# Optimization experiments

Measured on AMD Instinct MI355X. Metric: run time of the kernel, lower is better.

Reference implementation:

```python
import jax, jax.numpy as jnp
import numpy as np

B, N, K = 8, 2048, 100  # graphs per batch, nodes per graph, diffpool clusters


def _bn(x, g, b, eps=1e-5):
    # BatchNorm1d in training mode over all B*N nodes (biased variance)
    m = x.mean(axis=(0, 1))
    v = x.var(axis=(0, 1))
    return (x - m) * jax.lax.rsqrt(v + eps) * g + b


def _norm_adj(A):
    # PyG gcn_norm: add remaining self-loops (fill=1), D^-1/2 (A+I) D^-1/2
    n = A.shape[-1]
    d = jnp.diagonal(A, axis1=-2, axis2=-1)
    A_hat = A + jnp.where(d == 0, 1.0, 0.0)[..., :, None] * jnp.eye(n, dtype=A.dtype)
    deg = A_hat.sum(-1)
    dinv = jnp.where(deg > 0, 1.0 / jnp.sqrt(deg), 0.0)
    return dinv[..., :, None] * A_hat * dinv[..., None, :]


def _gcn(An, x, W, b):
    # GCNConv: propagate(x @ W) + bias, with pre-normalized adjacency
    return An @ (x @ W) + b


def _forward(x, adj, W_in, W3030, Wp13, b30, b100, Wfc_pool, bfc_pool,
             W1, b1, W2, b2, gamma30, beta30, gamma100, beta100):
    A_w = _norm_adj(adj)                               # weighted (edge_attr) adjacency
    A_b = _norm_adj((adj > 0).astype(adj.dtype))       # pool convs ignore edge_attr
    # feature branch
    x11 = _bn(_gcn(A_w, x, W_in[0], b30[0]), gamma30[0], beta30[0])
    x12 = _bn(_gcn(A_w, x11, W3030[0], b30[1]), gamma30[1], beta30[1])
    x13 = _bn(_gcn(A_w, x12, W3030[1], b30[2]), gamma30[2], beta30[2])
    x1_out = jnp.concatenate([x11, x12, x13], -1).max(axis=1)   # [B,90]
    # assignment branch
    s11 = _bn(_gcn(A_b, x, W_in[1], b30[3]), gamma30[3], beta30[3])
    s12 = _bn(_gcn(A_b, s11, W3030[2], b30[4]), gamma30[4], beta30[4])
    s13 = _bn(_gcn(A_b, s12, Wp13, b100), gamma100, beta100)
    s1 = jnp.concatenate([s11, s12, s13], -1) @ Wfc_pool + bfc_pool  # [B,N,K]
    # dense_diff_pool (link/entropy losses are unused by the forward output)
    s = jax.nn.softmax(s1, -1)
    p1_x = jnp.einsum('bnk,bnd->bkd', s, x13)          # s^T x  [B,K,30]
    p1_adj = jnp.einsum('bnk,bnl->bkl', s, adj @ s)    # s^T A s  [B,K,K]
    # second stage on pooled (dense, weighted) graph
    A2 = _norm_adj(p1_adj)
    x21 = _bn(_gcn(A2, p1_x, W3030[3], b30[5]), gamma30[5], beta30[5])
    x22 = _bn(_gcn(A2, x21, W3030[4], b30[6]), gamma30[6], beta30[6])
    x23 = _bn(_gcn(A2, x22, W3030[5], b30[7]), gamma30[7], beta30[7])
    x2_out = jnp.concatenate([x21, x22, x23], -1).max(axis=1)   # [B,90]
    h = jnp.concatenate([x1_out, x2_out], -1) @ W1 + b1
    return jax.nn.relu(h) @ W2 + b2                    # [B,6]


def setup_inputs():
    key = jax.random.key(0)
    ks = jax.random.split(key, 12)
    u = jax.random.uniform(ks[0], (B, N, N), dtype=jnp.float32)
    mask = jax.random.uniform(ks[1], (B, N, N)) < 0.05
    A = jnp.triu(u * mask, 1)
    adj = A + jnp.swapaxes(A, -1, -2)
    x = jax.random.normal(ks[2], (B, N, 3), dtype=jnp.float32)
    w = lambda k, s: jax.random.normal(k, s, dtype=jnp.float32) * 0.1
    return dict(
        x=x, adj=adj,
        W_in=w(ks[3], (2, 3, 30)),      # conv11, pool_conv11
        W3030=w(ks[4], (6, 30, 30)),    # conv12, conv13, pool_conv12, conv21..23
        Wp13=w(ks[5], (30, 100)),
        b30=jnp.zeros((8, 30), jnp.float32),
        b100=jnp.zeros((100,), jnp.float32),
        Wfc_pool=w(ks[6], (160, 100)), bfc_pool=jnp.zeros((100,), jnp.float32),
        W1=w(ks[7], (180, 50)), b1=jnp.zeros((50,), jnp.float32),
        W2=w(ks[8], (50, 6)), b2=jnp.zeros((6,), jnp.float32),
        gamma30=jnp.ones((8, 30), jnp.float32), beta30=jnp.zeros((8, 30), jnp.float32),
        gamma100=jnp.ones((100,), jnp.float32), beta100=jnp.zeros((100,), jnp.float32),
    )


def reference(x, adj, W_in, W3030, Wp13, b30, b100, Wfc_pool, bfc_pool,
              W1, b1, W2, b2, gamma30, beta30, gamma100, beta100):
    return _forward(x, adj, W_in, W3030, Wp13, b30, b100, Wfc_pool, bfc_pool,
                    W1, b1, W2, b2, gamma30, beta30, gamma100, beta100)
```

## Files before the change

kernel.cpp:

```cpp
#include <hip/hip_runtime.h>
#include <hip/hip_fp16.h>
#include <cstdint>
#include <cstddef>

#define BATCH 8
#define NN 2048
#define RTOT 16384
#define CAP 176

static constexpr size_t OF_B1W   = 0;
static constexpr size_t OF_B1B   = 3840;
static constexpr size_t OF_B2W   = 7680;
static constexpr size_t OF_B2B   = 11520;
static constexpr size_t OF_B3W   = 15360;
static constexpr size_t OF_B3B   = 15840;
static constexpr size_t OF_S2    = 17440;
static constexpr size_t OF_CNT   = 17620;
static constexpr size_t ZEND     = 17632;
static constexpr size_t OF_ELLV  = 17664;
static constexpr size_t OF_ELLC  = OF_ELLV + 2883584;
static constexpr size_t OF_ROWLEN= OF_ELLC + 1441792;
static constexpr size_t OF_DINVW = OF_ROWLEN + 16384;
static constexpr size_t OF_DINVB = OF_DINVW + 16384;
static constexpr size_t OF_HWB   = OF_DINVB + 16384;
static constexpr size_t OF_HW3   = OF_HWB + 524288;
static constexpr size_t OF_HB100 = OF_HW3 + 262144;
static constexpr size_t OF_ZW    = OF_HB100 + 851968;
static constexpr size_t OF_ZB    = OF_ZW + 524288;
static constexpr size_t OF_X11   = OF_ZB + 1703936;
static constexpr size_t OF_X12   = OF_X11 + 524288;
static constexpr size_t OF_X13   = OF_X12 + 524288;
static constexpr size_t OF_S11   = OF_X13 + 524288;
static constexpr size_t OF_S12   = OF_S11 + 524288;
static constexpr size_t OF_PARTMAX = OF_S12 + 524288;

#define FMA4(acc, s, h) { acc.x += (s)*(h).x; acc.y += (s)*(h).y; acc.z += (s)*(h).z; acc.w += (s)*(h).w; }

__device__ __forceinline__ unsigned short f2h(float f) {
  _Float16 h = (_Float16)f;
  return *(unsigned short*)&h;
}
__device__ __forceinline__ float h2f(unsigned short s) {
  _Float16 h = *(_Float16*)&s;
  return (float)h;
}
__device__ __forceinline__ float2 h2f2(unsigned int u) {
  __half2 h = *(__half2*)&u;
  return __half22float2(h);
}

struct __align__(8) us4 { unsigned short x, y, z, w; };

#define ACC8(g, wt) { \
  float2 f0=h2f2((g).x), f1=h2f2((g).y), f2=h2f2((g).z), f3=h2f2((g).w); \
  acc[0] += (wt)*f0.x; acc[1] += (wt)*f0.y; acc[2] += (wt)*f1.x; acc[3] += (wt)*f1.y; \
  acc[4] += (wt)*f2.x; acc[5] += (wt)*f2.y; acc[6] += (wt)*f3.x; acc[7] += (wt)*f3.y; }


__global__ __launch_bounds__(256) void k_build_ell(
    const float* __restrict__ adj, const float* __restrict__ x,
    const float* __restrict__ Win, float* __restrict__ ellv,
    unsigned short* __restrict__ ellc, int* __restrict__ rowlen,
    float* __restrict__ dinvw, float* __restrict__ dinvb,
    unsigned short* __restrict__ Hwb, float* __restrict__ zbase)
{
  int r = blockIdx.x;
  int t = threadIdx.x, lane = t & 63, wv = t >> 6;
  if (blockIdx.x < 69) {
    int zi = blockIdx.x * 256 + t;
    if (zi < (int)ZEND) zbase[zi] = 0.f;
  }
  const float* row = adj + (size_t)r * NN;
  __shared__ int wcnt[4];
  __shared__ float wsumA[4];
  __shared__ float dsh[2];
  float4 a = ((const float4*)row)[t];
  float4 b = ((const float4*)row)[256 + t];
  float vals[8] = {a.x, a.y, a.z, a.w, b.x, b.y, b.z, b.w};
  int cbase0 = t*4, cbase1 = 1024 + t*4;
  int cnt = 0; float sum = 0.f;
#pragma unroll
  for (int k = 0; k < 8; ++k) { sum += vals[k]; cnt += (vals[k] != 0.f) ? 1 : 0; }
  int pre = cnt;
#pragma unroll
  for (int o = 1; o < 64; o <<= 1) { int n = __shfl_up(pre, o); if (lane >= o) pre += n; }
  int excl = pre - cnt;
  int wtot = __shfl(pre, 63);
#pragma unroll
  for (int o = 32; o; o >>= 1) sum += __shfl_down(sum, o);
  if (lane == 0) { wcnt[wv] = wtot; wsumA[wv] = sum; }
  __syncthreads();
  int base = 0;
  for (int w = 0; w < wv; ++w) base += wcnt[w];
  int p = base + excl;
  size_t rb = (size_t)r * CAP;
#pragma unroll
  for (int k = 0; k < 8; ++k) {
    float v = vals[k];
    if (v != 0.f && p < CAP) {
      ellv[rb + p] = v;
      ellc[rb + p] = (unsigned short)((k < 4) ? (cbase0 + k) : (cbase1 + (k - 4)));
      ++p;
    }
  }
  if (t == 0) {
    int tot = wcnt[0] + wcnt[1] + wcnt[2] + wcnt[3];
    float ws = wsumA[0] + wsumA[1] + wsumA[2] + wsumA[3];
    int nnz = tot < CAP ? tot : CAP;
    int n = nnz;
    while ((n & 3) && n < CAP) { ellv[rb + n] = 0.f; ellc[rb + n] = 0; ++n; }
    rowlen[r] = n;
    float dw = rsqrtf(ws + 1.f), db = rsqrtf((float)nnz + 1.f);
    dinvw[r] = dw; dinvb[r] = db;
    dsh[0] = dw; dsh[1] = db;
  }
  __syncthreads();
  if (t < 64) {
    int c = t & 31, side = t >> 5;
    float v = 0.f;
    if (c < 30) {
      float x0 = x[r*3], x1 = x[r*3+1], x2 = x[r*3+2];
      const float* W = Win + side*90;
      v = (x0*W[c] + x1*W[30+c] + x2*W[60+c]) * dsh[side];
    }
    Hwb[(size_t)r*64 + t] = f2h(v);
  }
}

__global__ __launch_bounds__(256) void k_spmm_pair(
    const unsigned short* __restrict__ Hwb, const float* __restrict__ ellv,
    const unsigned short* __restrict__ ellc, const int* __restrict__ rowlen,
    const float* __restrict__ dinvw, const float* __restrict__ dinvb,
    float* __restrict__ Zw, float* __restrict__ Zb,
    float* __restrict__ bktW, float* __restrict__ bktB)
{
  __shared__ float zsW[32][32];
  __shared__ float zsB[32][32];
  int t = threadIdx.x;
  int gid = blockIdx.x * 256 + t;
  int row = gid >> 3, q = gid & 7;
  int side = q >> 2, sub = q & 3;
  int len = rowlen[row];
  const float4* ev = (const float4*)(ellv + (size_t)row * CAP);
  const uint2*  ec = (const uint2*) (ellc + (size_t)row * CAP);
  const uint4* HP = (const uint4*)(Hwb + (size_t)(row >> 11) * (NN*64));
  float acc[8] = {0,0,0,0,0,0,0,0};
  int nit = len >> 2;
  for (int i = 0; i < nit; ++i) {
    float4 v = ev[i];
    uint2 cc = ec[i];
    int c0 = cc.x & 0xffff, c1 = cc.x >> 16, c2 = cc.y & 0xffff, c3 = cc.y >> 16;
    uint4 g0 = HP[c0*8+q], g1 = HP[c1*8+q], g2 = HP[c2*8+q], g3 = HP[c3*8+q];
    float w0 = side ? (v.x>0.f?1.f:0.f) : v.x;
    float w1 = side ? (v.y>0.f?1.f:0.f) : v.y;
    float w2 = side ? (v.z>0.f?1.f:0.f) : v.z;
    float w3 = side ? (v.w>0.f?1.f:0.f) : v.w;
    ACC8(g0, w0); ACC8(g1, w1); ACC8(g2, w2); ACC8(g3, w3);
  }
  uint4 hs = HP[(row & (NN-1))*8 + q];
  ACC8(hs, 1.f);
  float d = side ? dinvb[row] : dinvw[row];
#pragma unroll
  for (int k = 0; k < 8; ++k) acc[k] *= d;
  float* Zp = (side ? Zb : Zw) + (size_t)row*32 + sub*8;
  float4 o0 = {acc[0],acc[1],acc[2],acc[3]}, o1 = {acc[4],acc[5],acc[6],acc[7]};
  ((float4*)Zp)[0] = o0; ((float4*)Zp)[1] = o1;
  int rowloc = t >> 3;
  float (*zs)[32] = side ? zsB : zsW;
#pragma unroll
  for (int k = 0; k < 8; ++k) zs[rowloc][sub*8+k] = acc[k];
  __syncthreads();
  int copy = blockIdx.x & 63;
  if (t < 30) {
    float s1 = 0.f, s2 = 0.f;
    for (int r = 0; r < 32; ++r) { float v = zsW[r][t]; s1 += v; s2 += v*v; }
    atomicAdd(&bktW[(t*64+copy)*2],   s1);
    atomicAdd(&bktW[(t*64+copy)*2+1], s2);
  } else if (t >= 64 && t < 94) {
    int c = t - 64;
    float s1 = 0.f, s2 = 0.f;
    for (int r = 0; r < 32; ++r) { float v = zsB[r][c]; s1 += v; s2 += v*v; }
    atomicAdd(&bktB[(c*64+copy)*2],   s1);
    atomicAdd(&bktB[(c*64+copy)*2+1], s2);
  }
}

__global__ __launch_bounds__(256) void k_spmm_l3(
    const unsigned short* __restrict__ Hw3, const unsigned short* __restrict__ Hb100,
    const float* __restrict__ ellv, const unsigned short* __restrict__ ellc,
    const int* __restrict__ rowlen, const float* __restrict__ dinvw,
    const float* __restrict__ dinvb, float* __restrict__ Zw, float* __restrict__ Zb,
    float* __restrict__ bktW3, float* __restrict__ bktB3)
{
  __shared__ float zs[64][32];
  __shared__ float st[200];
  int t = threadIdx.x;
  if (blockIdx.x < 256) {
    int gid = blockIdx.x * 256 + t;
    int row = gid >> 2, q = gid & 3;
    int len = rowlen[row];
    const float4* ev = (const float4*)(ellv + (size_t)row * CAP);
    const uint2*  ec = (const uint2*) (ellc + (size_t)row * CAP);
    const uint4* HP = (const uint4*)(Hw3 + (size_t)(row >> 11) * (NN*32));
    float acc[8] = {0,0,0,0,0,0,0,0};
    int nit = len >> 2;
    for (int i = 0; i < nit; ++i) {
      float4 v = ev[i];
      uint2 cc = ec[i];
      int c0 = cc.x & 0xffff, c1 = cc.x >> 16, c2 = cc.y & 0xffff, c3 = cc.y >> 16;
      uint4 g0 = HP[c0*4+q], g1 = HP[c1*4+q], g2 = HP[c2*4+q], g3 = HP[c3*4+q];
      ACC8(g0, v.x); ACC8(g1, v.y); ACC8(g2, v.z); ACC8(g3, v.w);
    }
    uint4 hs = HP[(row & (NN-1))*4 + q];
    ACC8(hs, 1.f);
    float d = dinvw[row];
#pragma unroll
    for (int k = 0; k < 8; ++k) acc[k] *= d;
    float* Zp = Zw + (size_t)row*32 + q*8;
    float4 o0 = {acc[0],acc[1],acc[2],acc[3]}, o1 = {acc[4],acc[5],acc[6],acc[7]};
    ((float4*)Zp)[0] = o0; ((float4*)Zp)[1] = o1;
    int rowloc = t >> 2;
#pragma unroll
    for (int k = 0; k < 8; ++k) zs[rowloc][q*8+k] = acc[k];
    __syncthreads();
    if (t < 30) {
      float s1 = 0.f, s2 = 0.f;
      for (int r = 0; r < 64; ++r) { float v = zs[r][t]; s1 += v; s2 += v*v; }
      int copy = blockIdx.x & 7;
      atomicAdd(&bktW3[(t*8+copy)*2],   s1);
      atomicAdd(&bktW3[(t*8+copy)*2+1], s2);
    }
  } else {
    int bid = blockIdx.x - 256;
    for (int i = t; i < 200; i += 256) st[i] = 0.f;
    __syncthreads();
    int gid = bid * 256 + t;
    int row = gid / 13, q = gid - row*13;
    int len = rowlen[row];
    const float4* ev = (const float4*)(ellv + (size_t)row * CAP);
    const uint2*  ec = (const uint2*) (ellc + (size_t)row * CAP);
    const uint4* HP = (const uint4*)(Hb100 + (size_t)(row >> 11) * ((size_t)NN*104));
    float acc[8] = {0,0,0,0,0,0,0,0};
    int nit = len >> 2;
    for (int i = 0; i < nit; ++i) {
      float4 v = ev[i];
      uint2 cc = ec[i];
      int c0 = cc.x & 0xffff, c1 = cc.x >> 16, c2 = cc.y & 0xffff, c3 = cc.y >> 16;
      uint4 g0 = HP[c0*13+q], g1 = HP[c1*13+q], g2 = HP[c2*13+q], g3 = HP[c3*13+q];
      float w0 = (v.x>0.f?1.f:0.f), w1 = (v.y>0.f?1.f:0.f);
      float w2 = (v.z>0.f?1.f:0.f), w3 = (v.w>0.f?1.f:0.f);
      ACC8(g0, w0); ACC8(g1, w1); ACC8(g2, w2); ACC8(g3, w3);
    }
    uint4 hs = HP[(row & (NN-1))*13 + q];
    ACC8(hs, 1.f);
    float d = dinvb[row];
#pragma unroll
    for (int k = 0; k < 8; ++k) acc[k] *= d;
    float* Zp = Zb + (size_t)row*104 + q*8;
    float4 o0 = {acc[0],acc[1],acc[2],acc[3]}, o1 = {acc[4],acc[5],acc[6],acc[7]};
    ((float4*)Zp)[0] = o0; ((float4*)Zp)[1] = o1;
    int c0 = q*8;
#pragma unroll
    for (int k = 0; k < 8; ++k) {
      int ch = c0 + k;
      if (ch < 100) { atomicAdd(&st[ch*2], acc[k]); atomicAdd(&st[ch*2+1], acc[k]*acc[k]); }
    }
    __syncthreads();
    int copy = bid & 7;
    for (int i = t; i < 200; i += 256)
      atomicAdd(&bktB3[((i>>1)*8 + copy)*2 + (i&1)], st[i]);
  }
}

template<int LEVEL>
__global__ __launch_bounds__(256) void k_apply_gemm(
    const float* __restrict__ Zw, const float* __restrict__ bktW,
    const float* __restrict__ gW, const float* __restrict__ beW,
    float* __restrict__ xst, const float* __restrict__ Ww,
    const float* __restrict__ dinvw,
    const float* __restrict__ Zb, const float* __restrict__ bktB,
    const float* __restrict__ gB, const float* __restrict__ beB,
    float* __restrict__ sst, const float* __restrict__ Wb,
    const float* __restrict__ dinvb,
    unsigned short* __restrict__ HwOut, unsigned short* __restrict__ HbOut)
{
  constexpr int NGB = (LEVEL == 1) ? 8 : 26;
  constexpr int OSTRIDEB = (LEVEL == 1) ? 32 : 104;
  constexpr int NG = 8 + NGB;
  __shared__ float WwL[30*32];
  __shared__ float WbL[30*OSTRIDEB];
  __shared__ float awL[60], abL[60];
  int t = threadIdx.x;
  if (t < 60) {
    int c = t % 30;
    bool isW = t < 30;
    const float4* p = (const float4*)((isW ? bktW : bktB) + c*128);
    float s1 = 0.f, s2 = 0.f;
#pragma unroll
    for (int k = 0; k < 32; ++k) { float4 v = p[k]; s1 += v.x + v.z; s2 += v.y + v.w; }
    float mean = s1/16384.f, var = s2/16384.f - mean*mean, inv = rsqrtf(var + 1e-5f);
    float aa = (isW ? gW : gB)[c]*inv;
    float* dst = isW ? awL : abL;
    dst[c] = aa; dst[30+c] = (isW ? beW : beB)[c] - mean*aa;
  }
  for (int idx = t; idx < 30*32; idx += 256) {
    int k = idx >> 5, c = idx & 31;
    WwL[idx] = (c < 30) ? Ww[k*30 + c] : 0.f;
  }
  if (LEVEL == 1) {
    for (int idx = t; idx < 30*32; idx += 256) {
      int k = idx >> 5, c = idx & 31;
      WbL[idx] = (c < 30) ? Wb[k*30 + c] : 0.f;
    }
  } else {
    for (int idx = t; idx < 30*OSTRIDEB; idx += 256) {
      int k = idx / OSTRIDEB, j = idx % OSTRIDEB;
      WbL[idx] = (j < 100) ? Wb[k*100 + j] : 0.f;
    }
  }
  __syncthreads();
  int gid = blockIdx.x * 256 + t;
  int row = gid / NG, g = gid % NG;
  if (g < 8) {
    const float4* Z4 = (const float4*)Zw + (size_t)row*8;
    float4 z4[8];
#pragma unroll
    for (int u = 0; u < 8; ++u) z4[u] = Z4[u];
    const float* z = (const float*)z4;
    float4 xv;
    int ch = 4*g;
    xv.x = (ch+0 < 30) ? awL[ch+0]*z[ch+0] + awL[30+ch+0] : 0.f;
    xv.y = (ch+1 < 30) ? awL[ch+1]*z[ch+1] + awL[30+ch+1] : 0.f;
    xv.z = (ch+2 < 30) ? awL[ch+2]*z[ch+2] + awL[30+ch+2] : 0.f;
    xv.w = (ch+3 < 30) ? awL[ch+3]*z[ch+3] + awL[30+ch+3] : 0.f;
    ((float4*)xst)[(size_t)row*8+g] = xv;
    float4 o = {0,0,0,0};
#pragma unroll
    for (int k = 0; k < 30; ++k) {
      float xk = awL[k]*z[k] + awL[30+k];
      float4 w = *(const float4*)(WwL + k*32 + 4*g);
      FMA4(o, xk, w);
    }
    float d = dinvw[row];
    us4 pv = { f2h(d*o.x), f2h(d*o.y), f2h(d*o.z), f2h(d*o.w) };
    unsigned short* dst = (LEVEL == 1) ? (HwOut + (size_t)row*64 + 4*g)
                                       : (HwOut + (size_t)row*32 + 4*g);
    *(us4*)dst = pv;
  } else {
    int gb = g - 8;
    const float4* Z4 = (const float4*)Zb + (size_t)row*8;
    float4 z4[8];
#pragma unroll
    for (int u = 0; u < 8; ++u) z4[u] = Z4[u];
    const float* z = (const float*)z4;
    if (gb < 8) {
      int ch = 4*gb;
      float4 sv;
      sv.x = (ch+0 < 30) ? abL[ch+0]*z[ch+0] + abL[30+ch+0] : 0.f;
      sv.y = (ch+1 < 30) ? abL[ch+1]*z[ch+1] + abL[30+ch+1] : 0.f;
      sv.z = (ch+2 < 30) ? abL[ch+2]*z[ch+2] + abL[30+ch+2] : 0.f;
      sv.w = (ch+3 < 30) ? abL[ch+3]*z[ch+3] + abL[30+ch+3] : 0.f;
      ((float4*)sst)[(size_t)row*8+gb] = sv;
    }
    float4 o = {0,0,0,0};
#pragma unroll
    for (int k = 0; k < 30; ++k) {
      float sk = abL[k]*z[k] + abL[30+k];
      float4 w = *(const float4*)(WbL + k*OSTRIDEB + 4*gb);
      FMA4(o, sk, w);
    }
    float d = dinvb[row];
    us4 pv = { f2h(d*o.x), f2h(d*o.y), f2h(d*o.z), f2h(d*o.w) };
    unsigned short* dst = (LEVEL == 1) ? (HbOut + (size_t)row*64 + 32 + 4*gb)
                                       : (HbOut + (size_t)row*104 + 4*gb);
    *(us4*)dst = pv;
  }
}

__global__ __launch_bounds__(256) void k_fcpool(
    const float* __restrict__ Zw3, const float* __restrict__ bktW3,
    const float* __restrict__ gW3, const float* __restrict__ beW3,
    const float* __restrict__ Zb3, const float* __restrict__ bktB3,
    const float* __restrict__ g100, const float* __restrict__ be100,
    const float* __restrict__ s11, const float* __restrict__ s12,
    const float* __restrict__ Wfc, const float* __restrict__ bfc,
    float* __restrict__ x13, unsigned short* __restrict__ S)
{
  __shared__ float shm[14240];
  __shared__ float aw3[60], ab3[200];
  float* feat = shm;
  float* Wl = shm + 10240;
  int t = threadIdx.x;
  int g0 = blockIdx.x * 64;
  if (t < 30) {
    const float4* p = (const float4*)(bktW3 + t*16);
    float s1 = 0.f, s2 = 0.f;
#pragma unroll
    for (int k = 0; k < 4; ++k) { float4 v = p[k]; s1 += v.x + v.z; s2 += v.y + v.w; }
    float mean = s1/16384.f, var = s2/16384.f - mean*mean, inv = rsqrtf(var + 1e-5f);
    float aa = gW3[t]*inv; aw3[t] = aa; aw3[30+t] = beW3[t] - mean*aa;
  } else if (t >= 64 && t < 164) {
    int c = t - 64;
    const float4* p = (const float4*)(bktB3 + c*16);
    float s1 = 0.f, s2 = 0.f;
#pragma unroll
    for (int k = 0; k < 4; ++k) { float4 v = p[k]; s1 += v.x + v.z; s2 += v.y + v.w; }
    float mean = s1/16384.f, var = s2/16384.f - mean*mean, inv = rsqrtf(var + 1e-5f);
    float aa = g100[c]*inv; ab3[c] = aa; ab3[100+c] = be100[c] - mean*aa;
  }
  __syncthreads();
  for (int idx = t; idx < 64*160; idx += 256) {
    int l = idx / 160, c = idx % 160;
    int g = g0 + l;
    float v;
    if (c < 30) v = s11[(size_t)g*32 + c];
    else if (c < 60) v = s12[(size_t)g*32 + (c-30)];
    else { int k = c - 60; v = ab3[k]*Zb3[(size_t)g*104 + k] + ab3[100 + k]; }
    feat[l*160 + c] = v;
  }
  for (int idx = t; idx < 64*32; idx += 256) {
    int l = idx >> 5, c = idx & 31;
    int g = g0 + l;
    x13[(size_t)g*32+c] = (c < 30) ? aw3[c]*Zw3[(size_t)g*32+c] + aw3[30+c] : 0.f;
  }
  int np = t >> 3, kg = t & 7;
  int n0 = np*2, n1 = np*2 + 1;
  int kbase = kg*12 + (kg < 4 ? kg : 4);
  int klen  = kg < 4 ? 13 : 12;
  float a0[13], a1[13];
#pragma unroll
  for (int j = 0; j < 13; ++j) { a0[j] = 0.f; a1[j] = 0.f; }
  for (int ch = 0; ch < 4; ++ch) {
    __syncthreads();
    for (int idx = t; idx < 4000; idx += 256) {
      int r = idx/100, j = idx%100;
      Wl[r*100 + j] = Wfc[(ch*40 + r)*100 + j];
    }
    __syncthreads();
    for (int kk = 0; kk < 40; ++kk) {
      float f0 = feat[n0*160 + ch*40+kk];
      float f1 = feat[n1*160 + ch*40+kk];
#pragma unroll
      for (int j = 0; j < 13; ++j) {
        if (j < klen) {
          float w = Wl[kk*100 + kbase + j];
          a0[j] += f0*w; a1[j] += f1*w;
        }
      }
    }
  }
  __syncthreads();
  float* sRow = shm;
  for (int j = 0; j < klen; ++j) {
    int k = kbase + j;
    sRow[n0*100 + k] = a0[j] + bfc[k];
    sRow[n1*100 + k] = a1[j] + bfc[k];
  }
  __syncthreads();
  int n = t >> 2, part = t & 3;
  int i0 = part*25;
  float m = -3.4e38f;
  for (int i = 0; i < 25; ++i) m = fmaxf(m, sRow[n*100 + i0 + i]);
  m = fmaxf(m, __shfl_xor(m, 1));
  m = fmaxf(m, __shfl_xor(m, 2));
  float ev[25]; float s = 0.f;
  for (int i = 0; i < 25; ++i) { float e = __expf(sRow[n*100 + i0 + i] - m); ev[i] = e; s += e; }
  s += __shfl_xor(s, 1);
  s += __shfl_xor(s, 2);
  float rinv = 1.f / s;
  for (int i = 0; i < 25; ++i) S[(size_t)(g0+n)*104 + i0 + i] = f2h(ev[i] * rinv);
  if (part == 3) {
    S[(size_t)(g0+n)*104 + 100] = 0; S[(size_t)(g0+n)*104 + 101] = 0;
    S[(size_t)(g0+n)*104 + 102] = 0; S[(size_t)(g0+n)*104 + 103] = 0;
  }
}

__global__ __launch_bounds__(256) void k_spmm_as(
    const unsigned short* __restrict__ S, const float* __restrict__ ellv,
    const unsigned short* __restrict__ ellc, const int* __restrict__ rowlen,
    float* __restrict__ Z)
{
  int t = threadIdx.x;
  int gid = blockIdx.x * 256 + t;
  int row = gid / 13, q = gid - row*13;
  int len = rowlen[row];
  const float4* ev = (const float4*)(ellv + (size_t)row * CAP);
  const uint2*  ec = (const uint2*) (ellc + (size_t)row * CAP);
  const uint4* HP = (const uint4*)(S + (size_t)(row >> 11) * ((size_t)NN*104));
  float acc[8] = {0,0,0,0,0,0,0,0};
  int nit = len >> 2;
  for (int i = 0; i < nit; ++i) {
    float4 v = ev[i];
    uint2 cc = ec[i];
    int c0 = cc.x & 0xffff, c1 = cc.x >> 16, c2 = cc.y & 0xffff, c3 = cc.y >> 16;
    uint4 g0 = HP[c0*13+q], g1 = HP[c1*13+q], g2 = HP[c2*13+q], g3 = HP[c3*13+q];
    ACC8(g0, v.x); ACC8(g1, v.y); ACC8(g2, v.z); ACC8(g3, v.w);
  }
  float* Zp = Z + (size_t)row*104 + q*8;
  float4 o0 = {acc[0],acc[1],acc[2],acc[3]}, o1 = {acc[4],acc[5],acc[6],acc[7]};
  ((float4*)Zp)[0] = o0; ((float4*)Zp)[1] = o1;
}

__global__ __launch_bounds__(256) void k_pool_part(
    const unsigned short* __restrict__ S, const float* __restrict__ x13,
    const float* __restrict__ As, const float* __restrict__ x11,
    const float* __restrict__ x12, float* __restrict__ pp, float* __restrict__ pm)
{
  __shared__ float sL[64][100];
  __shared__ float xL[64][132];
  __shared__ float red[256];
  int t = threadIdx.x;
  int b = blockIdx.x >> 3, chunk = blockIdx.x & 7;
  int g00 = b * 2048 + chunk * 256;
  int kt = t/10, dt = t%10;
  int k0 = kt*4, d0 = dt*13;
  float acc[4][13];
#pragma unroll
  for (int a = 0; a < 4; ++a)
#pragma unroll
    for (int j = 0; j < 13; ++j) acc[a][j] = 0.f;
  for (int tile = 0; tile < 4; ++tile) {
    int g0 = g00 + tile*64;
    __syncthreads();
    for (int idx = t; idx < 64*100; idx += 256) {
      int l = idx/100, k = idx%100;
      sL[l][k] = h2f(S[(size_t)(g0+l)*104 + k]);
    }
    for (int idx = t; idx < 64*130; idx += 256) {
      int l = idx/130, d = idx%130;
      xL[l][d] = d < 30 ? x13[(size_t)(g0+l)*32 + d] : As[(size_t)(g0+l)*104 + (d-30)];
    }
    __syncthreads();
    if (t < 250) {
      for (int kk = 0; kk < 64; ++kk) {
        float sv[4];
#pragma unroll
        for (int a = 0; a < 4; ++a) sv[a] = sL[kk][k0+a];
#pragma unroll
        for (int j = 0; j < 13; ++j) {
          float xv = xL[kk][d0+j];
#pragma unroll
          for (int a = 0; a < 4; ++a) acc[a][j] += sv[a]*xv;
        }
      }
    }
  }
  if (t < 250) {
    float* dst = pp + (size_t)blockIdx.x * 13000;
    for (int a = 0; a < 4; ++a)
      for (int j = 0; j < 13; ++j)
        dst[(k0+a)*130 + (d0+j)] = acc[a][j];
  }
  __syncthreads();
  {
    int c = t & 31, rg = t >> 5;
    const float* srcs[3] = {x11, x12, x13};
    for (int a = 0; a < 3; ++a) {
      const float* p = srcs[a] + (size_t)(g00+rg)*32 + c;
      float m = -3.4e38f;
      for (int it = 0; it < 32; ++it) m = fmaxf(m, p[it*256]);
      red[t] = m;
      __syncthreads();
      if (t < 30) {
        float mm = red[t];
        for (int g = 1; g < 8; ++g) mm = fmaxf(mm, red[g*32+t]);
        pm[(size_t)blockIdx.x*90 + a*30 + t] = mm;
      }
      __syncthreads();
    }
  }
}

__global__ __launch_bounds__(256) void k_s2fused(
    const float* __restrict__ pp, const float* __restrict__ partmax,
    const float* __restrict__ Wm,
    const float* __restrict__ g30,
    const float* __restrict__ be30,
    float* __restrict__ bktS2,
    int* __restrict__ cnt,
    const float* __restrict__ W1, const float* __restrict__ b1,
    const float* __restrict__ W2, const float* __restrict__ b2,
    float* __restrict__ out)
{
  __shared__ float A2f[10000];
  __shared__ float buf1[3000];
  __shared__ float buf2[3200];
  __shared__ float WL[960];
  __shared__ float dl[100];
  __shared__ float st1[30], st2[30];
  __shared__ float coef[60];
  __shared__ float x1L[90], x2L[90], hh[50];
  int b = blockIdx.x, t = threadIdx.x;
  for (int idx = t; idx < 13000; idx += 256) {
    float s = 0.f;
    for (int ch = 0; ch < 8; ++ch) s += pp[(size_t)(b*8 + ch)*13000 + idx];
    int k = idx/130, d = idx%130;
    if (d < 30) buf1[k*30 + d] = s;
    else A2f[k*100 + (d-30)] = s;
  }
  __syncthreads();
  if (t < 100 && A2f[t*101] == 0.f) A2f[t*101] = 1.f;
  __syncthreads();
  if (t < 100) {
    float s = 0.f;
    for (int j = 0; j < 100; ++j) s += A2f[t*100 + j];
    dl[t] = s > 0.f ? rsqrtf(s) : 0.f;
  }
  __syncthreads();
  for (int idx = t; idx < 10000; idx += 256) {
    int i = idx/100, j = idx%100;
    A2f[idx] = dl[i]*dl[j]*A2f[idx];
  }
  int rp = t >> 2, cg = t & 3;
  int i0 = rp*2, c0 = cg*8;
  bool act = (t < 200);
  for (int L = 0; L < 3; ++L) {
    if (t < 30) { st1[t] = 0.f; st2[t] = 0.f; }
    const float* W = Wm + L*900;
    for (int idx = t; idx < 960; idx += 256) {
      int k = idx >> 5, c = idx & 31;
      WL[idx] = (c < 30) ? W[k*30 + c] : 0.f;
    }
    __syncthreads();
    if (act) {
      float a0[8] = {0,0,0,0,0,0,0,0}, a1[8] = {0,0,0,0,0,0,0,0};
      for (int k = 0; k < 30; ++k) {
        float xx0 = buf1[i0*30 + k], xx1 = buf1[(i0+1)*30 + k];
        float4 w0 = *(const float4*)&WL[k*32 + c0];
        float4 w1 = *(const float4*)&WL[k*32 + c0 + 4];
        a0[0] += xx0*w0.x; a0[1] += xx0*w0.y; a0[2] += xx0*w0.z; a0[3] += xx0*w0.w;
        a0[4] += xx0*w1.x; a0[5] += xx0*w1.y; a0[6] += xx0*w1.z; a0[7] += xx0*w1.w;
        a1[0] += xx1*w0.x; a1[1] += xx1*w0.y; a1[2] += xx1*w0.z; a1[3] += xx1*w0.w;
        a1[4] += xx1*w1.x; a1[5] += xx1*w1.y; a1[6] += xx1*w1.z; a1[7] += xx1*w1.w;
      }
      float4 s00 = {a0[0],a0[1],a0[2],a0[3]}, s01 = {a0[4],a0[5],a0[6],a0[7]};
      float4 s10 = {a1[0],a1[1],a1[2],a1[3]}, s11v = {a1[4],a1[5],a1[6],a1[7]};
      *(float4*)&buf2[i0*32 + c0]       = s00;
      *(float4*)&buf2[i0*32 + c0 + 4]   = s01;
      *(float4*)&buf2[(i0+1)*32 + c0]   = s10;
      *(float4*)&buf2[(i0+1)*32 + c0+4] = s11v;
    }
    __syncthreads();
    if (act) {
      float z0[8] = {0,0,0,0,0,0,0,0}, z1[8] = {0,0,0,0,0,0,0,0};
      for (int j = 0; j < 100; ++j) {
        float av0 = A2f[i0*100 + j], av1 = A2f[(i0+1)*100 + j];
        float4 t0 = *(const float4*)&buf2[j*32 + c0];
        float4 t1 = *(const float4*)&buf2[j*32 + c0 + 4];
        z0[0] += av0*t0.x; z0[1] += av0*t0.y; z0[2] += av0*t0.z; z0[3] += av0*t0.w;
        z0[4] += av0*t1.x; z0[5] += av0*t1.y; z0[6] += av0*t1.z; z0[7] += av0*t1.w;
        z1[0] += av1*t0.x; z1[1] += av1*t0.y; z1[2] += av1*t0.z; z1[3] += av1*t0.w;
        z1[4] += av1*t1.x; z1[5] += av1*t1.y; z1[6] += av1*t1.z; z1[7] += av1*t1.w;
      }
#pragma unroll
      for (int k = 0; k < 8; ++k) {
        int c = c0 + k;
        if (c < 30) {
          buf1[i0*30 + c]     = z0[k];
          buf1[(i0+1)*30 + c] = z1[k];
          atomicAdd(&st1[c], z0[k] + z1[k]);
          atomicAdd(&st2[c], z0[k]*z0[k] + z1[k]*z1[k]);
        }
      }
    }
    __syncthreads();
    if (t < 30) {
      atomicAdd(&bktS2[(L*30+t)*2],   st1[t]);
      atomicAdd(&bktS2[(L*30+t)*2+1], st2[t]);
    }
    __syncthreads();
    if (t == 0) {
      __threadfence();
      atomicAdd(cnt, 1);
      while (atomicAdd(cnt, 0) < (L+1)*8) {}
      __threadfence();
    }
    __syncthreads();
    if (t < 30) {
      float s1 = atomicAdd(&bktS2[(L*30+t)*2],   0.f);
      float s2 = atomicAdd(&bktS2[(L*30+t)*2+1], 0.f);
      float mean = s1/800.f, var = s2/800.f - mean*mean, inv = rsqrtf(var + 1e-5f);
      float aa = g30[L*30+t]*inv;
      coef[t] = aa; coef[30+t] = be30[L*30+t] - mean*aa;
    }
    __syncthreads();
    if (L < 2) {
      for (int idx = t; idx < 3000; idx += 256) {
        int c = idx % 30;
        buf1[idx] = coef[c]*buf1[idx] + coef[30+c];
      }
      __syncthreads();
      if (t < 30) {
        float m = -3.4e38f;
        for (int i = 0; i < 100; ++i) m = fmaxf(m, buf1[i*30+t]);
        x2L[L*30+t] = m;
      }
      __syncthreads();
    } else {
      if (t < 30) {
        float m = -3.4e38f;
        for (int i = 0; i < 100; ++i) m = fmaxf(m, coef[t]*buf1[i*30+t] + coef[30+t]);
        x2L[60+t] = m;
      }
    }
  }
  if (t < 90) {
    float m = -3.4e38f;
    for (int s = 0; s < 8; ++s) m = fmaxf(m, partmax[(size_t)(b*8+s)*90 + t]);
    x1L[t] = m;
  }
  __syncthreads();
  if (t < 50) {
    float a = b1[t];
    for (int k = 0; k < 90; ++k) a += x1L[k]*W1[k*50+t];
    for (int k = 0; k < 90; ++k) a += x2L[k]*W1[(90+k)*50+t];
    hh[t] = fmaxf(a, 0.f);
  }
  __syncthreads();
  if (t < 6) {
    float a = b2[t];
    for (int j = 0; j < 50; ++j) a += hh[j]*W2[j*6+t];
    out[b*6+t] = a;
  }
}

extern "C" void kernel_launch(void* const* d_in, const int* in_sizes, int n_in,
                              void* d_out, int out_size, void* d_ws, size_t ws_size,
                              hipStream_t stream)
{
  const float* x    = (const float*)d_in[0];
  const float* adj  = (const float*)d_in[1];
  const float* Win  = (const float*)d_in[2];
  const float* W3030= (const float*)d_in[3];
  const float* Wp13 = (const float*)d_in[4];
  const float* Wfc  = (const float*)d_in[7];
  const float* bfc  = (const float*)d_in[8];
  const float* W1   = (const float*)d_in[9];
  const float* b1   = (const float*)d_in[10];
  const float* W2   = (const float*)d_in[11];
  const float* b2   = (const float*)d_in[12];
  const float* g30  = (const float*)d_in[13];
  const float* be30 = (const float*)d_in[14];
  const float* g100 = (const float*)d_in[15];
  const float* be100= (const float*)d_in[16];
  float* out = (float*)d_out;

  float* wsf = (float*)d_ws;
  float* bL1W = wsf + OF_B1W;  float* bL1B = wsf + OF_B1B;
  float* bL2W = wsf + OF_B2W;  float* bL2B = wsf + OF_B2B;
  float* bL3W = wsf + OF_B3W;  float* bL3B = wsf + OF_B3B;
  float* bktS2 = wsf + OF_S2;
  int*   cnt  = (int*)(wsf + OF_CNT);
  float* ellv  = wsf + OF_ELLV;
  unsigned short* ellc = (unsigned short*)(wsf + OF_ELLC);
  int*   rowlen = (int*)(wsf + OF_ROWLEN);
  float* dinvw = wsf + OF_DINVW;
  float* dinvb = wsf + OF_DINVB;
  unsigned short* Hwb   = (unsigned short*)(wsf + OF_HWB);
  unsigned short* Hw3   = (unsigned short*)(wsf + OF_HW3);
  unsigned short* Hb100 = (unsigned short*)(wsf + OF_HB100);
  unsigned short* S     = Hb100;
  float* Zw = wsf + OF_ZW;
  float* Zb = wsf + OF_ZB;
  float* x11 = wsf + OF_X11;
  float* x12 = wsf + OF_X12;
  float* x13 = wsf + OF_X13;
  float* s11 = wsf + OF_S11;
  float* s12 = wsf + OF_S12;
  float* pp  = wsf + OF_S11;
  float* partmax = wsf + OF_PARTMAX;

  k_build_ell<<<RTOT, 256, 0, stream>>>(adj, x, Win, ellv, ellc, rowlen, dinvw, dinvb, Hwb, wsf);

  k_spmm_pair<<<512, 256, 0, stream>>>(Hwb, ellv, ellc, rowlen, dinvw, dinvb, Zw, Zb, bL1W, bL1B);
  k_apply_gemm<1><<<1024, 256, 0, stream>>>(Zw, bL1W, g30+0, be30+0, x11, W3030+0, dinvw,
                                            Zb, bL1B, g30+90, be30+90, s11, W3030+2*900, dinvb, Hwb, Hwb);

  k_spmm_pair<<<512, 256, 0, stream>>>(Hwb, ellv, ellc, rowlen, dinvw, dinvb, Zw, Zb, bL2W, bL2B);
  k_apply_gemm<2><<<2176, 256, 0, stream>>>(Zw, bL2W, g30+30, be30+30, x12, W3030+900, dinvw,
                                            Zb, bL2B, g30+120, be30+120, s12, Wp13, dinvb, Hw3, Hb100);

  k_spmm_l3<<<1088, 256, 0, stream>>>(Hw3, Hb100, ellv, ellc, rowlen, dinvw, dinvb, Zw, Zb, bL3W, bL3B);
  k_fcpool<<<256, 256, 0, stream>>>(Zw, bL3W, g30+60, be30+60, Zb, bL3B, g100, be100,
                                    s11, s12, Wfc, bfc, x13, S);

  k_spmm_as<<<832, 256, 0, stream>>>(S, ellv, ellc, rowlen, Zb );
  k_pool_part<<<64, 256, 0, stream>>>(S, x13, Zb, x11, x12, pp, partmax);

  k_s2fused<<<BATCH, 256, 0, stream>>>(pp, partmax, W3030+3*900, g30+150, be30+150,
                                       bktS2, cnt, W1, b1, W2, b2, out);
}
```

Baseline: 658.9 us.

## Split pooling into more blocks with separate reduce kernel, unroll SpMM gathers by two

The pooling partial-product kernel now uses 256 blocks of 64 rows each instead of 64 blocks looping over four tiles. This fills more compute units, and a new reduction kernel sums the 32 partials per graph before the final fused kernel. The SpMM gather loops in several kernels are unrolled by two to keep eight independent gathers in flight. The cost is an extra launch, a larger partials buffer in the workspace, and higher register pressure.

```diff
diff --git a/kernel.cpp b/kernel.cpp
--- a/kernel.cpp
+++ b/kernel.cpp
@@ -33,6 +33,8 @@
 static constexpr size_t OF_S11   = OF_X13 + 524288;
 static constexpr size_t OF_S12   = OF_S11 + 524288;
 static constexpr size_t OF_PARTMAX = OF_S12 + 524288;
+static constexpr size_t OF_PP    = OF_PARTMAX + 23040;
+static constexpr size_t OF_PPOOL = OF_PP + 3328000;
 
 #define FMA4(acc, s, h) { acc.x += (s)*(h).x; acc.y += (s)*(h).y; acc.z += (s)*(h).z; acc.w += (s)*(h).w; }
 
@@ -146,7 +148,26 @@
   const uint4* HP = (const uint4*)(Hwb + (size_t)(row >> 11) * (NN*64));
   float acc[8] = {0,0,0,0,0,0,0,0};
   int nit = len >> 2;
-  for (int i = 0; i < nit; ++i) {
+  int i = 0;
+  for (; i + 2 <= nit; i += 2) {
+    float4 v0 = ev[i], v1 = ev[i+1];
+    uint2 cc0 = ec[i], cc1 = ec[i+1];
+    int a0 = cc0.x & 0xffff, a1 = cc0.x >> 16, a2 = cc0.y & 0xffff, a3 = cc0.y >> 16;
+    int e0 = cc1.x & 0xffff, e1 = cc1.x >> 16, e2 = cc1.y & 0xffff, e3 = cc1.y >> 16;
+    uint4 g0 = HP[a0*8+q], g1 = HP[a1*8+q], g2 = HP[a2*8+q], g3 = HP[a3*8+q];
+    uint4 g4 = HP[e0*8+q], g5 = HP[e1*8+q], g6 = HP[e2*8+q], g7 = HP[e3*8+q];
+    float w0 = side ? (v0.x>0.f?1.f:0.f) : v0.x;
+    float w1 = side ? (v0.y>0.f?1.f:0.f) : v0.y;
+    float w2 = side ? (v0.z>0.f?1.f:0.f) : v0.z;
+    float w3 = side ? (v0.w>0.f?1.f:0.f) : v0.w;
+    float w4 = side ? (v1.x>0.f?1.f:0.f) : v1.x;
+    float w5 = side ? (v1.y>0.f?1.f:0.f) : v1.y;
+    float w6 = side ? (v1.z>0.f?1.f:0.f) : v1.z;
+    float w7 = side ? (v1.w>0.f?1.f:0.f) : v1.w;
+    ACC8(g0, w0); ACC8(g1, w1); ACC8(g2, w2); ACC8(g3, w3);
+    ACC8(g4, w4); ACC8(g5, w5); ACC8(g6, w6); ACC8(g7, w7);
+  }
+  if (i < nit) {
     float4 v = ev[i];
     uint2 cc = ec[i];
     int c0 = cc.x & 0xffff, c1 = cc.x >> 16, c2 = cc.y & 0xffff, c3 = cc.y >> 16;
@@ -204,7 +225,18 @@
     const uint4* HP = (const uint4*)(Hw3 + (size_t)(row >> 11) * (NN*32));
     float acc[8] = {0,0,0,0,0,0,0,0};
     int nit = len >> 2;
-    for (int i = 0; i < nit; ++i) {
+    int i = 0;
+    for (; i + 2 <= nit; i += 2) {
+      float4 v0 = ev[i], v1 = ev[i+1];
+      uint2 cc0 = ec[i], cc1 = ec[i+1];
+      int a0 = cc0.x & 0xffff, a1 = cc0.x >> 16, a2 = cc0.y & 0xffff, a3 = cc0.y >> 16;
+      int e0 = cc1.x & 0xffff, e1 = cc1.x >> 16, e2 = cc1.y & 0xffff, e3 = cc1.y >> 16;
+      uint4 g0 = HP[a0*4+q], g1 = HP[a1*4+q], g2 = HP[a2*4+q], g3 = HP[a3*4+q];
+      uint4 g4 = HP[e0*4+q], g5 = HP[e1*4+q], g6 = HP[e2*4+q], g7 = HP[e3*4+q];
+      ACC8(g0, v0.x); ACC8(g1, v0.y); ACC8(g2, v0.z); ACC8(g3, v0.w);
+      ACC8(g4, v1.x); ACC8(g5, v1.y); ACC8(g6, v1.z); ACC8(g7, v1.w);
+    }
+    if (i < nit) {
       float4 v = ev[i];
       uint2 cc = ec[i];
       int c0 = cc.x & 0xffff, c1 = cc.x >> 16, c2 = cc.y & 0xffff, c3 = cc.y >> 16;
@@ -242,7 +274,22 @@
     const uint4* HP = (const uint4*)(Hb100 + (size_t)(row >> 11) * ((size_t)NN*104));
     float acc[8] = {0,0,0,0,0,0,0,0};
     int nit = len >> 2;
-    for (int i = 0; i < nit; ++i) {
+    int i = 0;
+    for (; i + 2 <= nit; i += 2) {
+      float4 v0 = ev[i], v1 = ev[i+1];
+      uint2 cc0 = ec[i], cc1 = ec[i+1];
+      int a0 = cc0.x & 0xffff, a1 = cc0.x >> 16, a2 = cc0.y & 0xffff, a3 = cc0.y >> 16;
+      int e0 = cc1.x & 0xffff, e1 = cc1.x >> 16, e2 = cc1.y & 0xffff, e3 = cc1.y >> 16;
+      uint4 g0 = HP[a0*13+q], g1 = HP[a1*13+q], g2 = HP[a2*13+q], g3 = HP[a3*13+q];
+      uint4 g4 = HP[e0*13+q], g5 = HP[e1*13+q], g6 = HP[e2*13+q], g7 = HP[e3*13+q];
+      float w0 = (v0.x>0.f?1.f:0.f), w1 = (v0.y>0.f?1.f:0.f);
+      float w2 = (v0.z>0.f?1.f:0.f), w3 = (v0.w>0.f?1.f:0.f);
+      float w4 = (v1.x>0.f?1.f:0.f), w5 = (v1.y>0.f?1.f:0.f);
+      float w6 = (v1.z>0.f?1.f:0.f), w7 = (v1.w>0.f?1.f:0.f);
+      ACC8(g0, w0); ACC8(g1, w1); ACC8(g2, w2); ACC8(g3, w3);
+      ACC8(g4, w4); ACC8(g5, w5); ACC8(g6, w6); ACC8(g7, w7);
+    }
+    if (i < nit) {
       float4 v = ev[i];
       uint2 cc = ec[i];
       int c0 = cc.x & 0xffff, c1 = cc.x >> 16, c2 = cc.y & 0xffff, c3 = cc.y >> 16;
@@ -267,8 +314,8 @@
     }
     __syncthreads();
     int copy = bid & 7;
-    for (int i = t; i < 200; i += 256)
-      atomicAdd(&bktB3[((i>>1)*8 + copy)*2 + (i&1)], st[i]);
+    for (int i2 = t; i2 < 200; i2 += 256)
+      atomicAdd(&bktB3[((i2>>1)*8 + copy)*2 + (i2&1)], st[i2]);
   }
 }
 
@@ -327,12 +374,13 @@
 #pragma unroll
     for (int u = 0; u < 8; ++u) z4[u] = Z4[u];
     const float* z = (const float*)z4;
+    int ch = 4*g;
+    float4 zg = Z4[g];
     float4 xv;
-    int ch = 4*g;
-    xv.x = (ch+0 < 30) ? awL[ch+0]*z[ch+0] + awL[30+ch+0] : 0.f;
-    xv.y = (ch+1 < 30) ? awL[ch+1]*z[ch+1] + awL[30+ch+1] : 0.f;
-    xv.z = (ch+2 < 30) ? awL[ch+2]*z[ch+2] + awL[30+ch+2] : 0.f;
-    xv.w = (ch+3 < 30) ? awL[ch+3]*z[ch+3] + awL[30+ch+3] : 0.f;
+    xv.x = (ch+0 < 30) ? awL[ch+0]*zg.x + awL[30+ch+0] : 0.f;
+    xv.y = (ch+1 < 30) ? awL[ch+1]*zg.y + awL[30+ch+1] : 0.f;
+    xv.z = (ch+2 < 30) ? awL[ch+2]*zg.z + awL[30+ch+2] : 0.f;
+    xv.w = (ch+3 < 30) ? awL[ch+3]*zg.w + awL[30+ch+3] : 0.f;
     ((float4*)xst)[(size_t)row*8+g] = xv;
     float4 o = {0,0,0,0};
 #pragma unroll
@@ -355,11 +403,12 @@
     const float* z = (const float*)z4;
     if (gb < 8) {
       int ch = 4*gb;
+      float4 zg = Z4[gb];
       float4 sv;
-      sv.x = (ch+0 < 30) ? abL[ch+0]*z[ch+0] + abL[30+ch+0] : 0.f;
-      sv.y = (ch+1 < 30) ? abL[ch+1]*z[ch+1] + abL[30+ch+1] : 0.f;
-      sv.z = (ch+2 < 30) ? abL[ch+2]*z[ch+2] + abL[30+ch+2] : 0.f;
-      sv.w = (ch+3 < 30) ? abL[ch+3]*z[ch+3] + abL[30+ch+3] : 0.f;
+      sv.x = (ch+0 < 30) ? abL[ch+0]*zg.x + abL[30+ch+0] : 0.f;
+      sv.y = (ch+1 < 30) ? abL[ch+1]*zg.y + abL[30+ch+1] : 0.f;
+      sv.z = (ch+2 < 30) ? abL[ch+2]*zg.z + abL[30+ch+2] : 0.f;
+      sv.w = (ch+3 < 30) ? abL[ch+3]*zg.w + abL[30+ch+3] : 0.f;
       ((float4*)sst)[(size_t)row*8+gb] = sv;
     }
     float4 o = {0,0,0,0};
@@ -489,7 +538,18 @@
   const uint4* HP = (const uint4*)(S + (size_t)(row >> 11) * ((size_t)NN*104));
   float acc[8] = {0,0,0,0,0,0,0,0};
   int nit = len >> 2;
-  for (int i = 0; i < nit; ++i) {
+  int i = 0;
+  for (; i + 2 <= nit; i += 2) {
+    float4 v0 = ev[i], v1 = ev[i+1];
+    uint2 cc0 = ec[i], cc1 = ec[i+1];
+    int a0 = cc0.x & 0xffff, a1 = cc0.x >> 16, a2 = cc0.y & 0xffff, a3 = cc0.y >> 16;
+    int e0 = cc1.x & 0xffff, e1 = cc1.x >> 16, e2 = cc1.y & 0xffff, e3 = cc1.y >> 16;
+    uint4 g0 = HP[a0*13+q], g1 = HP[a1*13+q], g2 = HP[a2*13+q], g3 = HP[a3*13+q];
+    uint4 g4 = HP[e0*13+q], g5 = HP[e1*13+q], g6 = HP[e2*13+q], g7 = HP[e3*13+q];
+    ACC8(g0, v0.x); ACC8(g1, v0.y); ACC8(g2, v0.z); ACC8(g3, v0.w);
+    ACC8(g4, v1.x); ACC8(g5, v1.y); ACC8(g6, v1.z); ACC8(g7, v1.w);
+  }
+  if (i < nit) {
     float4 v = ev[i];
     uint2 cc = ec[i];
     int c0 = cc.x & 0xffff, c1 = cc.x >> 16, c2 = cc.y & 0xffff, c3 = cc.y >> 16;
@@ -510,8 +570,8 @@
   __shared__ float xL[64][132];
   __shared__ float red[256];
   int t = threadIdx.x;
-  int b = blockIdx.x >> 3, chunk = blockIdx.x & 7;
-  int g00 = b * 2048 + chunk * 256;
+  int b = blockIdx.x >> 5, chunk = blockIdx.x & 31;
+  int g0 = b * 2048 + chunk * 64;
   int kt = t/10, dt = t%10;
   int k0 = kt*4, d0 = dt*13;
   float acc[4][13];
@@ -519,33 +579,27 @@
   for (int a = 0; a < 4; ++a)
 #pragma unroll
     for (int j = 0; j < 13; ++j) acc[a][j] = 0.f;
-  for (int tile = 0; tile < 4; ++tile) {
-    int g0 = g00 + tile*64;
-    __syncthreads();
-    for (int idx = t; idx < 64*100; idx += 256) {
-      int l = idx/100, k = idx%100;
-      sL[l][k] = h2f(S[(size_t)(g0+l)*104 + k]);
-    }
-    for (int idx = t; idx < 64*130; idx += 256) {
-      int l = idx/130, d = idx%130;
-      xL[l][d] = d < 30 ? x13[(size_t)(g0+l)*32 + d] : As[(size_t)(g0+l)*104 + (d-30)];
-    }
-    __syncthreads();
-    if (t < 250) {
-      for (int kk = 0; kk < 64; ++kk) {
-        float sv[4];
-#pragma unroll
-        for (int a = 0; a < 4; ++a) sv[a] = sL[kk][k0+a];
-#pragma unroll
-        for (int j = 0; j < 13; ++j) {
-          float xv = xL[kk][d0+j];
-#pragma unroll
-          for (int a = 0; a < 4; ++a) acc[a][j] += sv[a]*xv;
-        }
+  for (int idx = t; idx < 64*100; idx += 256) {
+    int l = idx/100, k = idx%100;
+    sL[l][k] = h2f(S[(size_t)(g0+l)*104 + k]);
+  }
+  for (int idx = t; idx < 64*130; idx += 256) {
+    int l = idx/130, d = idx%130;
+    xL[l][d] = d < 30 ? x13[(size_t)(g0+l)*32 + d] : As[(size_t)(g0+l)*104 + (d-30)];
+  }
+  __syncthreads();
+  if (t < 250) {
+    for (int kk = 0; kk < 64; ++kk) {
+      float sv[4];
+#pragma unroll
+      for (int a = 0; a < 4; ++a) sv[a] = sL[kk][k0+a];
+#pragma unroll
+      for (int j = 0; j < 13; ++j) {
+        float xv = xL[kk][d0+j];
+#pragma unroll
+        for (int a = 0; a < 4; ++a) acc[a][j] += sv[a]*xv;
       }
     }
-  }
-  if (t < 250) {
     float* dst = pp + (size_t)blockIdx.x * 13000;
     for (int a = 0; a < 4; ++a)
       for (int j = 0; j < 13; ++j)
@@ -555,10 +609,12 @@
   {
     int c = t & 31, rg = t >> 5;
     const float* srcs[3] = {x11, x12, x13};
+#pragma unroll
     for (int a = 0; a < 3; ++a) {
-      const float* p = srcs[a] + (size_t)(g00+rg)*32 + c;
+      const float* p = srcs[a] + (size_t)(g0+rg)*32 + c;
       float m = -3.4e38f;
-      for (int it = 0; it < 32; ++it) m = fmaxf(m, p[it*256]);
+#pragma unroll
+      for (int it = 0; it < 8; ++it) m = fmaxf(m, p[it*256]);
       red[t] = m;
       __syncthreads();
       if (t < 30) {
@@ -571,8 +627,22 @@
   }
 }
 
+__global__ __launch_bounds__(256) void k_pool_reduce(
+    const float* __restrict__ pp, float* __restrict__ ppool)
+{
+  int b = blockIdx.x / 51, blk = blockIdx.x % 51;
+  int idx = blk * 256 + threadIdx.x;
+  if (idx < 13000) {
+    const float* src = pp + (size_t)b * 32 * 13000 + idx;
+    float s = 0.f;
+#pragma unroll
+    for (int c = 0; c < 32; ++c) s += src[c*13000];
+    ppool[(size_t)b*13000 + idx] = s;
+  }
+}
+
 __global__ __launch_bounds__(256) void k_s2fused(
-    const float* __restrict__ pp, const float* __restrict__ partmax,
+    const float* __restrict__ ppool, const float* __restrict__ partmax,
     const float* __restrict__ Wm,
     const float* __restrict__ g30,
     const float* __restrict__ be30,
@@ -592,8 +662,7 @@
   __shared__ float x1L[90], x2L[90], hh[50];
   int b = blockIdx.x, t = threadIdx.x;
   for (int idx = t; idx < 13000; idx += 256) {
-    float s = 0.f;
-    for (int ch = 0; ch < 8; ++ch) s += pp[(size_t)(b*8 + ch)*13000 + idx];
+    float s = ppool[(size_t)b*13000 + idx];
     int k = idx/130, d = idx%130;
     if (d < 30) buf1[k*30 + d] = s;
     else A2f[k*100 + (d-30)] = s;
@@ -706,7 +775,7 @@
   }
   if (t < 90) {
     float m = -3.4e38f;
-    for (int s = 0; s < 8; ++s) m = fmaxf(m, partmax[(size_t)(b*8+s)*90 + t]);
+    for (int s = 0; s < 32; ++s) m = fmaxf(m, partmax[(size_t)(b*32+s)*90 + t]);
     x1L[t] = m;
   }
   __syncthreads();
@@ -767,7 +836,8 @@
   float* x13 = wsf + OF_X13;
   float* s11 = wsf + OF_S11;
   float* s12 = wsf + OF_S12;
-  float* pp  = wsf + OF_S11;
+  float* pp  = wsf + OF_PP;
+  float* ppool = wsf + OF_PPOOL;
   float* partmax = wsf + OF_PARTMAX;
 
   k_build_ell<<<RTOT, 256, 0, stream>>>(adj, x, Win, ellv, ellc, rowlen, dinvw, dinvb, Hwb, wsf);
@@ -785,8 +855,9 @@
                                     s11, s12, Wfc, bfc, x13, S);
 
   k_spmm_as<<<832, 256, 0, stream>>>(S, ellv, ellc, rowlen, Zb );
-  k_pool_part<<<64, 256, 0, stream>>>(S, x13, Zb, x11, x12, pp, partmax);
-
-  k_s2fused<<<BATCH, 256, 0, stream>>>(pp, partmax, W3030+3*900, g30+150, be30+150,
+  k_pool_part<<<256, 256, 0, stream>>>(S, x13, Zb, x11, x12, pp, partmax);
+  k_pool_reduce<<<408, 256, 0, stream>>>(pp, ppool);
+
+  k_s2fused<<<BATCH, 256, 0, stream>>>(ppool, partmax, W3030+3*900, g30+150, be30+150,
                                        bktS2, cnt, W1, b1, W2, b2, out);
 }
```

New measurement: 549.0 us. 1.2x faster.
